# Optimization experiments

Hardware: AMD Instinct MI355X
Metric: run time of the kernel (lower is better)

Reference implementation:

```python
import jax, jax.numpy as jnp
import numpy as np

D_MODEL = 1024
EXPANSION = 4
NUM_TILES = 4
D_FF = D_MODEL * EXPANSION


def setup_inputs() -> dict:
    key = jax.random.key(0)
    k1, k2, k3, k4, k5 = jax.random.split(key, 5)
    x = jax.random.normal(k1, (8, 2048, D_MODEL), dtype=jnp.float32)
    w_up = jax.random.normal(k2, (D_FF, D_MODEL), dtype=jnp.float32) * 0.02
    b_up = jax.random.normal(k3, (D_FF,), dtype=jnp.float32) * 0.02
    w_down = jax.random.normal(k4, (D_MODEL, D_FF), dtype=jnp.float32) * 0.02
    b_down = jax.random.normal(k5, (D_MODEL,), dtype=jnp.float32) * 0.02
    return {"x": x, "w_up": w_up, "b_up": b_up, "w_down": w_down, "b_down": b_down}


def reference(x, w_up, b_up, w_down, b_down):
    B, T, C = x.shape
    xf = x.reshape(B * T, C)  # [N, d_model]
    N = B * T

    # Emergent tile signatures: sign of per-tile row sums of up_proj weight.
    tile_up = D_FF // NUM_TILES
    signatures = jnp.sign(w_up.reshape(NUM_TILES, tile_up, C).sum(axis=1))  # [num_tiles, d_model]

    # Routing: argmax over input-signature alignment -> one-hot gate.
    scores = xf @ signatures.T                      # [N, num_tiles]
    winner = jnp.argmax(scores, axis=-1)            # [N]
    gate = jax.nn.one_hot(winner, NUM_TILES, dtype=xf.dtype)  # [N, num_tiles]

    # Tile-gated up projection (gate scales output tile blocks), then ReLU.
    hidden = xf @ w_up.T + b_up                     # [N, d_ff]
    hidden = (hidden.reshape(N, NUM_TILES, tile_up) * gate[:, :, None]).reshape(N, D_FF)
    hidden = jax.nn.relu(hidden)

    # Tile-gated down projection.
    tile_down = D_MODEL // NUM_TILES
    out = hidden @ w_down.T + b_down                # [N, d_model]
    out = (out.reshape(N, NUM_TILES, tile_down) * gate[:, :, None]).reshape(N, D_MODEL)

    return out.reshape(B, T, D_MODEL), gate.reshape(B, T, NUM_TILES)
```

## Files before the change

kernel.cpp:

```cpp
#include <hip/hip_runtime.h>
#include <stdint.h>
#include <stddef.h>

#define N_TOK 16384
#define DM    1024
#define DFF   4096
#define NT    4
#define TU    1024
#define TD    256

typedef __attribute__((ext_vector_type(8))) short  short8;
typedef __attribute__((ext_vector_type(4))) short  short4v;
typedef __attribute__((ext_vector_type(4))) float  floatx4;

__device__ inline unsigned short f2bf(float f){
  union { float f; uint32_t u; } v; v.f = f;
  uint32_t u = v.u + 0x7FFFu + ((v.u >> 16) & 1u);
  return (unsigned short)(u >> 16);
}

__device__ __forceinline__ void gll16(const void* g, void* l){
  __builtin_amdgcn_global_load_lds(
      (const __attribute__((address_space(1))) unsigned int*)g,
      (__attribute__((address_space(3))) unsigned int*)l,
      16, 0, 0);
}

__global__ void k_sig_partial(const float* __restrict__ w_up,
                              float* __restrict__ partial,
                              unsigned short* __restrict__ wupb){
  const int b = blockIdx.x, tid = threadIdx.x;
  const int tile = b >> 6, chunk = b & 63;
  const int c0 = tid * 4;
  const int row0 = tile*TU + chunk*16;
  float s0=0.f, s1=0.f, s2=0.f, s3=0.f;
  const float* base = w_up + (size_t)row0 * DM + c0;
  #pragma unroll
  for (int r = 0; r < 16; ++r){
    floatx4 v = *(const floatx4*)(base + (size_t)r * DM);
    s0 += v[0]; s1 += v[1]; s2 += v[2]; s3 += v[3];
    short4v p;
    p[0]=(short)f2bf(v[0]); p[1]=(short)f2bf(v[1]);
    p[2]=(short)f2bf(v[2]); p[3]=(short)f2bf(v[3]);
    *(short4v*)(wupb + (size_t)(row0 + r) * DM + c0) = p;
  }
  float* p = partial + ((size_t)tile*DM + c0) * 64 + chunk;
  p[0] = s0; p[64] = s1; p[128] = s2; p[192] = s3;
}

__global__ void k_sig_final(const float* __restrict__ partial,
                            float* __restrict__ sig){
  const int g = blockIdx.x * 256 + threadIdx.x;
  const float* p = partial + (size_t)g * 64;
  float s = 0.f;
  #pragma unroll
  for (int i = 0; i < 64; ++i) s += p[i];
  sig[g] = (s > 0.f) ? 1.f : ((s < 0.f) ? -1.f : 0.f);
}

__global__ void k_wdown_conv(const float* __restrict__ w,
                             unsigned short* __restrict__ wb){
  const size_t i = ((size_t)blockIdx.x * 256 + threadIdx.x) * 8;
  floatx4 v0 = *(const floatx4*)(w + i);
  floatx4 v1 = *(const floatx4*)(w + i + 4);
  short8 p;
  p[0]=(short)f2bf(v0[0]); p[1]=(short)f2bf(v0[1]); p[2]=(short)f2bf(v0[2]); p[3]=(short)f2bf(v0[3]);
  p[4]=(short)f2bf(v1[0]); p[5]=(short)f2bf(v1[1]); p[6]=(short)f2bf(v1[2]); p[7]=(short)f2bf(v1[3]);
  *(short8*)(wb + i) = p;
}

__global__ __launch_bounds__(256) void k_route(
    const float* __restrict__ x, const float* __restrict__ sig,
    float* __restrict__ gate_out, int* __restrict__ winner,
    unsigned short* __restrict__ xbf){
  __shared__ float ssig[NT * DM];
  const int tid = threadIdx.x;
  for (int i = tid; i < NT*DM; i += 256) ssig[i] = sig[i];
  __syncthreads();
  const int wv = tid >> 6, lane = tid & 63;
  const int n = blockIdx.x * 4 + wv;
  const float* xr = x + (size_t)n * DM;
  unsigned short* xb = xbf + (size_t)n * 2048 + 1024;
  double a0=0.0, a1=0.0, a2=0.0, a3=0.0;
  #pragma unroll
  for (int j = 0; j < 4; ++j){
    const int c = j*256 + lane*4;
    floatx4 v = *(const floatx4*)(xr + c);
    short4v p;
    p[0]=(short)f2bf(v[0]); p[1]=(short)f2bf(v[1]);
    p[2]=(short)f2bf(v[2]); p[3]=(short)f2bf(v[3]);
    *(short4v*)(xb + c) = p;
    #pragma unroll
    for (int u = 0; u < 4; ++u){
      double xv = (double)v[u];
      a0 += xv * (double)ssig[c+u];
      a1 += xv * (double)ssig[DM   + c+u];
      a2 += xv * (double)ssig[2*DM + c+u];
      a3 += xv * (double)ssig[3*DM + c+u];
    }
  }
  #pragma unroll
  for (int off = 32; off > 0; off >>= 1){
    a0 += __shfl_down(a0, off, 64);
    a1 += __shfl_down(a1, off, 64);
    a2 += __shfl_down(a2, off, 64);
    a3 += __shfl_down(a3, off, 64);
  }
  if (lane == 0){
    double s[4] = {a0, a1, a2, a3};
    int w = 0;
    #pragma unroll
    for (int t = 1; t < 4; ++t) if (s[t] > s[w]) w = t;
    floatx4 g = { w==0 ? 1.f:0.f, w==1 ? 1.f:0.f, w==2 ? 1.f:0.f, w==3 ? 1.f:0.f };
    *(floatx4*)(gate_out + (size_t)n * 4) = g;
    winner[n] = w;
  }
}

__global__ void k_hist(const int* __restrict__ winner,
                       int* __restrict__ blk_cnt){
  __shared__ int wcnt[4][NT];
  const int tid = threadIdx.x, wv = tid >> 6, lane = tid & 63;
  const int w = winner[blockIdx.x * 256 + tid];
  #pragma unroll
  for (int t = 0; t < NT; ++t){
    unsigned long long m = __ballot(w == t);
    if (lane == 0) wcnt[wv][t] = __popcll(m);
  }
  __syncthreads();
  if (tid < NT){
    int s = wcnt[0][tid] + wcnt[1][tid] + wcnt[2][tid] + wcnt[3][tid];
    blk_cnt[blockIdx.x * NT + tid] = s;
  }
}

__global__ void k_scan(const int* __restrict__ blk_cnt,
                       int* __restrict__ meta, int* __restrict__ blk_base){
  __shared__ int s[256];
  const int tid = threadIdx.x;
  s[tid] = blk_cnt[tid];
  __syncthreads();
  if (tid == 0){
    int tot[NT] = {0,0,0,0};
    for (int b = 0; b < 64; ++b)
      for (int t = 0; t < NT; ++t) tot[t] += s[b*NT + t];
    int off = 0, base[NT];
    for (int t = 0; t < NT; ++t){ meta[t] = tot[t]; meta[4+t] = off; base[t] = off; off += tot[t]; }
    for (int b = 0; b < 64; ++b)
      for (int t = 0; t < NT; ++t){ int c = s[b*NT + t]; s[b*NT + t] = base[t]; base[t] += c; }
  }
  __syncthreads();
  blk_base[tid] = s[tid];
}

__global__ void k_scatter(const int* __restrict__ winner,
                          const int* __restrict__ blk_base,
                          int* __restrict__ idx){
  __shared__ int wcnt[4][NT];
  const int tid = threadIdx.x, wv = tid >> 6, lane = tid & 63;
  const int n = blockIdx.x * 256 + tid;
  const int w = winner[n];
  unsigned long long mymask = 0;
  #pragma unroll
  for (int t = 0; t < NT; ++t){
    unsigned long long m = __ballot(w == t);
    if (lane == 0) wcnt[wv][t] = __popcll(m);
    if (t == w) mymask = m;
  }
  __syncthreads();
  const unsigned long long below = (lane == 0) ? 0ull : (~0ull >> (64 - lane));
  int pos = blk_base[blockIdx.x * NT + w] + __popcll(mymask & below);
  for (int v = 0; v < wv; ++v) pos += wcnt[v][w];
  idx[pos] = n;
}

__global__ __launch_bounds__(256, 2) void k_gemm1(
    const unsigned short* __restrict__ xbf,
    const unsigned short* __restrict__ wupb,
    const float* __restrict__ b_up, const int* __restrict__ meta,
    const int* __restrict__ idx, unsigned short* __restrict__ hid){
  const int tile = blockIdx.z;
  const int cnt  = meta[tile];
  const int p0   = blockIdx.x * 128;
  if (p0 >= cnt) return;
  const int off  = meta[4 + tile];
  const int nb   = blockIdx.y;

  __shared__ unsigned short smem[16384];
  unsigned short* As0 = smem;
  unsigned short* As1 = smem + 4096;
  unsigned short* Bs0 = smem + 8192;
  unsigned short* Bs1 = smem + 12288;
  __shared__ int nrow[128];

  const int tid = threadIdx.x;
  if (tid < 128){
    int p = p0 + tid;
    nrow[tid] = idx[off + (p < cnt ? p : cnt - 1)];
  }
  __syncthreads();

  const int wv = tid >> 6, lane = tid & 63;
  const int wm = (wv >> 1) * 64, wn = (wv & 1) * 64;
  const int l16 = lane & 15, quad = lane >> 4;

  const int rsub = lane >> 2;
  const int kus  = (lane & 3) * 8;

  const int ra = wv*32 + rsub;
  const unsigned short* aptr0 = xbf + (size_t)nrow[ra]      * 2048 + 1024 + kus;
  const unsigned short* aptr1 = xbf + (size_t)nrow[ra + 16] * 2048 + 1024 + kus;
  const unsigned short* bptr0 = wupb + (size_t)(tile*TU + nb*128 + wv*32 + rsub) * DM + kus;
  const unsigned short* bptr1 = bptr0 + 16 * DM;

  unsigned short* a0d0 = As0 + (wv*32) * 32;  unsigned short* a0d1 = a0d0 + 16*32;
  unsigned short* a1d0 = As1 + (wv*32) * 32;  unsigned short* a1d1 = a1d0 + 16*32;
  unsigned short* b0d0 = Bs0 + (wv*32) * 32;  unsigned short* b0d1 = b0d0 + 16*32;
  unsigned short* b1d0 = Bs1 + (wv*32) * 32;  unsigned short* b1d1 = b1d0 + 16*32;

  floatx4 acc[4][4];
  #pragma unroll
  for (int i = 0; i < 4; ++i)
    #pragma unroll
    for (int j = 0; j < 4; ++j) acc[i][j] = (floatx4){0.f,0.f,0.f,0.f};

  for (int k0 = 0; k0 < DM; k0 += 64){
    gll16(aptr0 + k0,      a0d0);
    gll16(aptr1 + k0,      a0d1);
    gll16(aptr0 + k0 + 32, a1d0);
    gll16(aptr1 + k0 + 32, a1d1);
    gll16(bptr0 + k0,      b0d0);
    gll16(bptr1 + k0,      b0d1);
    gll16(bptr0 + k0 + 32, b1d0);
    gll16(bptr1 + k0 + 32, b1d1);
    __syncthreads();
    {
      short8 af[4], bfr[4];
      #pragma unroll
      for (int i = 0; i < 4; ++i) af[i]  = *(const short8*)(As0 + (wm + i*16 + l16)*32 + quad*8);
      #pragma unroll
      for (int j = 0; j < 4; ++j) bfr[j] = *(const short8*)(Bs0 + (wn + j*16 + l16)*32 + quad*8);
      #pragma unroll
      for (int i = 0; i < 4; ++i)
        #pragma unroll
        for (int j = 0; j < 4; ++j)
          acc[i][j] = __builtin_amdgcn_mfma_f32_16x16x32_bf16(af[i], bfr[j], acc[i][j], 0, 0, 0);
    }
    {
      short8 af[4], bfr[4];
      #pragma unroll
      for (int i = 0; i < 4; ++i) af[i]  = *(const short8*)(As1 + (wm + i*16 + l16)*32 + quad*8);
      #pragma unroll
      for (int j = 0; j < 4; ++j) bfr[j] = *(const short8*)(Bs1 + (wn + j*16 + l16)*32 + quad*8);
      #pragma unroll
      for (int i = 0; i < 4; ++i)
        #pragma unroll
        for (int j = 0; j < 4; ++j)
          acc[i][j] = __builtin_amdgcn_mfma_f32_16x16x32_bf16(af[i], bfr[j], acc[i][j], 0, 0, 0);
    }
    __syncthreads();
  }

  const int gcol0 = nb*128;
  #pragma unroll
  for (int half = 0; half < 2; ++half){
    if ((wv >> 1) == half){
      #pragma unroll
      for (int i = 0; i < 4; ++i){
        #pragma unroll
        for (int j = 0; j < 4; ++j){
          const int col = wn + j*16 + l16;
          const float bias = b_up[tile*TU + gcol0 + col];
          #pragma unroll
          for (int r = 0; r < 4; ++r){
            const int lrow = i*16 + quad*4 + r;
            float v = acc[i][j][r] + bias;
            smem[lrow*136 + col] = f2bf(v > 0.f ? v : 0.f);
          }
        }
      }
    }
    __syncthreads();
    #pragma unroll
    for (int c = tid; c < 1024; c += 256){
      const int lrow = c >> 4, k8 = (c & 15) * 8;
      const int m = half*64 + lrow;
      if (p0 + m < cnt){
        short8 vv = *(const short8*)(smem + lrow*136 + k8);
        *(short8*)(hid + (size_t)nrow[m]*2048 + gcol0 + k8) = vv;
      }
    }
    __syncthreads();
  }
}

__global__ __launch_bounds__(256, 2) void k_gemm2(
    const unsigned short* __restrict__ hid,
    const unsigned short* __restrict__ wdownb,
    const float* __restrict__ b_down, const int* __restrict__ meta,
    const int* __restrict__ idx, float* __restrict__ out){
  const int tile = blockIdx.z;
  const int cnt  = meta[tile];
  const int p0   = blockIdx.x * 32;
  if (p0 >= cnt) return;
  const int off  = meta[4 + tile];

  __shared__ unsigned short smem[18432];
  unsigned short* As0 = smem;
  unsigned short* As1 = smem + 1024;
  unsigned short* Bs0 = smem + 2048;
  unsigned short* Bs1 = smem + 10240;
  float* epi = (float*)smem;
  __shared__ int nrow[32];

  const int tid = threadIdx.x;
  if (tid < 32){
    int p = p0 + tid;
    nrow[tid] = idx[off + (p < cnt ? p : cnt - 1)];
  }
  __syncthreads();

  const int wv = tid >> 6, lane = tid & 63;
  const int wn = wv * 64;
  const int l16 = lane & 15, quad = lane >> 4;

  const int rsub = lane >> 2;
  const int kus  = (lane & 3) * 8;

  const int arow = (wv & 1)*16 + rsub;
  const unsigned short* aptr = hid + (size_t)nrow[arow] * 2048 + kus;
  const int aoff = (wv >> 1) * 32;
  unsigned short* asd = (wv < 2 ? As0 : As1) + ((wv & 1)*16) * 32;
  const unsigned short* bptr = wdownb + (size_t)(tile*TD + wv*64 + rsub) * DFF + tile*TU + kus;
  unsigned short* bsd0 = Bs0 + (wv*64) * 32;
  unsigned short* bsd1 = Bs1 + (wv*64) * 32;

  floatx4 acc[2][4];
  #pragma unroll
  for (int i = 0; i < 2; ++i)
    #pragma unroll
    for (int j = 0; j < 4; ++j) acc[i][j] = (floatx4){0.f,0.f,0.f,0.f};

  for (int k0 = 0; k0 < TU; k0 += 64){
    gll16(aptr + k0 + aoff, asd);
    gll16(bptr + k0,               bsd0);
    gll16(bptr + k0 + 16*DFF,      bsd0 + 16*32);
    gll16(bptr + k0 + 32*DFF,      bsd0 + 32*32);
    gll16(bptr + k0 + 48*DFF,      bsd0 + 48*32);
    gll16(bptr + k0 + 32,          bsd1);
    gll16(bptr + k0 + 32 + 16*DFF, bsd1 + 16*32);
    gll16(bptr + k0 + 32 + 32*DFF, bsd1 + 32*32);
    gll16(bptr + k0 + 32 + 48*DFF, bsd1 + 48*32);
    __syncthreads();
    {
      short8 af[2], bfr[4];
      #pragma unroll
      for (int i = 0; i < 2; ++i) af[i]  = *(const short8*)(As0 + (i*16 + l16)*32 + quad*8);
      #pragma unroll
      for (int j = 0; j < 4; ++j) bfr[j] = *(const short8*)(Bs0 + (wn + j*16 + l16)*32 + quad*8);
      #pragma unroll
      for (int i = 0; i < 2; ++i)
        #pragma unroll
        for (int j = 0; j < 4; ++j)
          acc[i][j] = __builtin_amdgcn_mfma_f32_16x16x32_bf16(af[i], bfr[j], acc[i][j], 0, 0, 0);
    }
    {
      short8 af[2], bfr[4];
      #pragma unroll
      for (int i = 0; i < 2; ++i) af[i]  = *(const short8*)(As1 + (i*16 + l16)*32 + quad*8);
      #pragma unroll
      for (int j = 0; j < 4; ++j) bfr[j] = *(const short8*)(Bs1 + (wn + j*16 + l16)*32 + quad*8);
      #pragma unroll
      for (int i = 0; i < 2; ++i)
        #pragma unroll
        for (int j = 0; j < 4; ++j)
          acc[i][j] = __builtin_amdgcn_mfma_f32_16x16x32_bf16(af[i], bfr[j], acc[i][j], 0, 0, 0);
    }
    __syncthreads();
  }

  const floatx4 z4 = {0.f, 0.f, 0.f, 0.f};
  #pragma unroll
  for (int cb = 0; cb < 4; ++cb){
    if (cb == tile) continue;
    for (int c = tid; c < 32*64; c += 256){
      const int rowl = c >> 6, c4 = (c & 63) * 4;
      if (p0 + rowl < cnt)
        *(floatx4*)(out + (size_t)nrow[rowl]*DM + cb*256 + c4) = z4;
    }
  }

  #pragma unroll
  for (int half = 0; half < 2; ++half){
    #pragma unroll
    for (int j = 0; j < 4; ++j){
      const int col = wn + j*16 + l16;
      const float bias = b_down[tile*TD + col];
      #pragma unroll
      for (int r = 0; r < 4; ++r){
        const int lrow = quad*4 + r;
        epi[lrow*260 + col] = acc[half][j][r] + bias;
      }
    }
    __syncthreads();
    #pragma unroll
    for (int c = tid; c < 1024; c += 256){
      const int lrow = c >> 6, c4 = (c & 63) * 4;
      const int m = half*16 + lrow;
      if (p0 + m < cnt){
        floatx4 v = *(const floatx4*)(epi + lrow*260 + c4);
        *(floatx4*)(out + (size_t)nrow[m]*DM + tile*TD + c4) = v;
      }
    }
    __syncthreads();
  }
}

extern "C" void kernel_launch(void* const* d_in, const int* in_sizes, int n_in,
                              void* d_out, int out_size, void* d_ws, size_t ws_size,
                              hipStream_t stream){
  const float* x      = (const float*)d_in[0];
  const float* w_up   = (const float*)d_in[1];
  const float* b_up   = (const float*)d_in[2];
  const float* w_down = (const float*)d_in[3];
  const float* b_down = (const float*)d_in[4];

  unsigned short* wupb   = (unsigned short*)d_ws;
  unsigned short* wdownb = wupb + (size_t)DFF * DM;
  float* partial = (float*)(wdownb + (size_t)DM * DFF);
  float* sig     = partial + 262144;
  int*   ints    = (int*)(sig + 4096);
  int*   winner   = ints;
  int*   idx      = ints + 16384;
  int*   meta     = ints + 32768;
  int*   blk_cnt  = ints + 32776;
  int*   blk_base = ints + 33032;

  float*          out  = (float*)d_out;
  float*          gate = out + (size_t)N_TOK * DM;
  unsigned short* ob16 = (unsigned short*)d_out;

  k_sig_partial<<<dim3(NT*64), 256, 0, stream>>>(w_up, partial, wupb);
  k_sig_final  <<<dim3(16),    256, 0, stream>>>(partial, sig);
  k_wdown_conv <<<dim3(2048),  256, 0, stream>>>(w_down, wdownb);
  k_route      <<<dim3(N_TOK/4), 256, 0, stream>>>(x, sig, gate, winner, ob16);
  k_hist       <<<dim3(64),    256, 0, stream>>>(winner, blk_cnt);
  k_scan       <<<dim3(1),     256, 0, stream>>>(blk_cnt, meta, blk_base);
  k_scatter    <<<dim3(64),    256, 0, stream>>>(winner, blk_base, idx);
  k_gemm1      <<<dim3(128, 8, NT), 256, 0, stream>>>(ob16, wupb, b_up, meta, idx, ob16);
  k_gemm2      <<<dim3(512, 1, NT), 256, 0, stream>>>(ob16, wdownb, b_down, meta, idx, out);
}
```

Before: 273.5 us.

## Fuse routing histogram/scan/scatter into route kernel via atomics and merge weight prep

New measurement: 274.0 us. No clear change (+0.2%).

```diff
diff --git a/kernel.cpp b/kernel.cpp
--- a/kernel.cpp
+++ b/kernel.cpp
@@ -26,10 +26,23 @@
       16, 0, 0);
 }
 
-__global__ void k_sig_partial(const float* __restrict__ w_up,
-                              float* __restrict__ partial,
-                              unsigned short* __restrict__ wupb){
-  const int b = blockIdx.x, tid = threadIdx.x;
+__global__ void k_prep(const float* __restrict__ w_up,
+                       const float* __restrict__ w_down,
+                       float* __restrict__ partial,
+                       unsigned short* __restrict__ wupb,
+                       unsigned short* __restrict__ wdownb){
+  const int tid = threadIdx.x;
+  if (blockIdx.x >= 256){
+    const size_t i = ((size_t)(blockIdx.x - 256) * 256 + tid) * 8;
+    floatx4 v0 = *(const floatx4*)(w_down + i);
+    floatx4 v1 = *(const floatx4*)(w_down + i + 4);
+    short8 p;
+    p[0]=(short)f2bf(v0[0]); p[1]=(short)f2bf(v0[1]); p[2]=(short)f2bf(v0[2]); p[3]=(short)f2bf(v0[3]);
+    p[4]=(short)f2bf(v1[0]); p[5]=(short)f2bf(v1[1]); p[6]=(short)f2bf(v1[2]); p[7]=(short)f2bf(v1[3]);
+    *(short8*)(wdownb + i) = p;
+    return;
+  }
+  const int b = blockIdx.x;
   const int tile = b >> 6, chunk = b & 63;
   const int c0 = tid * 4;
   const int row0 = tile*TU + chunk*16;
@@ -49,7 +62,9 @@
 }
 
 __global__ void k_sig_final(const float* __restrict__ partial,
-                            float* __restrict__ sig){
+                            float* __restrict__ sig,
+                            int* __restrict__ meta){
+  if (blockIdx.x == 0 && threadIdx.x < 8) meta[threadIdx.x] = 0;
   const int g = blockIdx.x * 256 + threadIdx.x;
   const float* p = partial + (size_t)g * 64;
   float s = 0.f;
@@ -58,132 +73,92 @@
   sig[g] = (s > 0.f) ? 1.f : ((s < 0.f) ? -1.f : 0.f);
 }
 
-__global__ void k_wdown_conv(const float* __restrict__ w,
-                             unsigned short* __restrict__ wb){
-  const size_t i = ((size_t)blockIdx.x * 256 + threadIdx.x) * 8;
-  floatx4 v0 = *(const floatx4*)(w + i);
-  floatx4 v1 = *(const floatx4*)(w + i + 4);
-  short8 p;
-  p[0]=(short)f2bf(v0[0]); p[1]=(short)f2bf(v0[1]); p[2]=(short)f2bf(v0[2]); p[3]=(short)f2bf(v0[3]);
-  p[4]=(short)f2bf(v1[0]); p[5]=(short)f2bf(v1[1]); p[6]=(short)f2bf(v1[2]); p[7]=(short)f2bf(v1[3]);
-  *(short8*)(wb + i) = p;
-}
-
 __global__ __launch_bounds__(256) void k_route(
     const float* __restrict__ x, const float* __restrict__ sig,
-    float* __restrict__ gate_out, int* __restrict__ winner,
-    unsigned short* __restrict__ xbf){
+    float* __restrict__ gate_out, int* __restrict__ meta,
+    int* __restrict__ idx4, unsigned short* __restrict__ xbf){
   __shared__ float ssig[NT * DM];
+  __shared__ int swin[16];
+  __shared__ int sbase[NT];
   const int tid = threadIdx.x;
   for (int i = tid; i < NT*DM; i += 256) ssig[i] = sig[i];
   __syncthreads();
   const int wv = tid >> 6, lane = tid & 63;
-  const int n = blockIdx.x * 4 + wv;
-  const float* xr = x + (size_t)n * DM;
-  unsigned short* xb = xbf + (size_t)n * 2048 + 1024;
-  double a0=0.0, a1=0.0, a2=0.0, a3=0.0;
+
+  floatx4 sg[4][4];
   #pragma unroll
   for (int j = 0; j < 4; ++j){
     const int c = j*256 + lane*4;
-    floatx4 v = *(const floatx4*)(xr + c);
-    short4v p;
-    p[0]=(short)f2bf(v[0]); p[1]=(short)f2bf(v[1]);
-    p[2]=(short)f2bf(v[2]); p[3]=(short)f2bf(v[3]);
-    *(short4v*)(xb + c) = p;
-    #pragma unroll
-    for (int u = 0; u < 4; ++u){
-      double xv = (double)v[u];
-      a0 += xv * (double)ssig[c+u];
-      a1 += xv * (double)ssig[DM   + c+u];
-      a2 += xv * (double)ssig[2*DM + c+u];
-      a3 += xv * (double)ssig[3*DM + c+u];
-    }
-  }
-  #pragma unroll
-  for (int off = 32; off > 0; off >>= 1){
-    a0 += __shfl_down(a0, off, 64);
-    a1 += __shfl_down(a1, off, 64);
-    a2 += __shfl_down(a2, off, 64);
-    a3 += __shfl_down(a3, off, 64);
-  }
-  if (lane == 0){
-    double s[4] = {a0, a1, a2, a3};
-    int w = 0;
-    #pragma unroll
-    for (int t = 1; t < 4; ++t) if (s[t] > s[w]) w = t;
-    floatx4 g = { w==0 ? 1.f:0.f, w==1 ? 1.f:0.f, w==2 ? 1.f:0.f, w==3 ? 1.f:0.f };
-    *(floatx4*)(gate_out + (size_t)n * 4) = g;
-    winner[n] = w;
-  }
-}
-
-__global__ void k_hist(const int* __restrict__ winner,
-                       int* __restrict__ blk_cnt){
-  __shared__ int wcnt[4][NT];
-  const int tid = threadIdx.x, wv = tid >> 6, lane = tid & 63;
-  const int w = winner[blockIdx.x * 256 + tid];
-  #pragma unroll
-  for (int t = 0; t < NT; ++t){
-    unsigned long long m = __ballot(w == t);
-    if (lane == 0) wcnt[wv][t] = __popcll(m);
+    #pragma unroll
+    for (int tt = 0; tt < 4; ++tt)
+      sg[j][tt] = *(const floatx4*)(ssig + tt*DM + c);
+  }
+
+  #pragma unroll
+  for (int t = 0; t < 4; ++t){
+    const int n = blockIdx.x * 16 + wv * 4 + t;
+    const float* xr = x + (size_t)n * DM;
+    unsigned short* xb = xbf + (size_t)n * 2048 + 1024;
+    double a0=0.0, a1=0.0, a2=0.0, a3=0.0;
+    #pragma unroll
+    for (int j = 0; j < 4; ++j){
+      const int c = j*256 + lane*4;
+      floatx4 v = *(const floatx4*)(xr + c);
+      short4v p;
+      p[0]=(short)f2bf(v[0]); p[1]=(short)f2bf(v[1]);
+      p[2]=(short)f2bf(v[2]); p[3]=(short)f2bf(v[3]);
+      *(short4v*)(xb + c) = p;
+      #pragma unroll
+      for (int u = 0; u < 4; ++u){
+        double xv = (double)v[u];
+        a0 += xv * (double)sg[j][0][u];
+        a1 += xv * (double)sg[j][1][u];
+        a2 += xv * (double)sg[j][2][u];
+        a3 += xv * (double)sg[j][3][u];
+      }
+    }
+    #pragma unroll
+    for (int off = 32; off > 0; off >>= 1){
+      a0 += __shfl_down(a0, off, 64);
+      a1 += __shfl_down(a1, off, 64);
+      a2 += __shfl_down(a2, off, 64);
+      a3 += __shfl_down(a3, off, 64);
+    }
+    if (lane == 0){
+      double s[4] = {a0, a1, a2, a3};
+      int w = 0;
+      #pragma unroll
+      for (int tt = 1; tt < 4; ++tt) if (s[tt] > s[w]) w = tt;
+      floatx4 g = { w==0 ? 1.f:0.f, w==1 ? 1.f:0.f, w==2 ? 1.f:0.f, w==3 ? 1.f:0.f };
+      *(floatx4*)(gate_out + (size_t)n * 4) = g;
+      swin[wv*4 + t] = w;
+    }
   }
   __syncthreads();
   if (tid < NT){
-    int s = wcnt[0][tid] + wcnt[1][tid] + wcnt[2][tid] + wcnt[3][tid];
-    blk_cnt[blockIdx.x * NT + tid] = s;
-  }
-}
-
-__global__ void k_scan(const int* __restrict__ blk_cnt,
-                       int* __restrict__ meta, int* __restrict__ blk_base){
-  __shared__ int s[256];
-  const int tid = threadIdx.x;
-  s[tid] = blk_cnt[tid];
+    int c = 0;
+    #pragma unroll
+    for (int i = 0; i < 16; ++i) c += (swin[i] == tid) ? 1 : 0;
+    sbase[tid] = atomicAdd(&meta[tid], c);
+  }
   __syncthreads();
-  if (tid == 0){
-    int tot[NT] = {0,0,0,0};
-    for (int b = 0; b < 64; ++b)
-      for (int t = 0; t < NT; ++t) tot[t] += s[b*NT + t];
-    int off = 0, base[NT];
-    for (int t = 0; t < NT; ++t){ meta[t] = tot[t]; meta[4+t] = off; base[t] = off; off += tot[t]; }
-    for (int b = 0; b < 64; ++b)
-      for (int t = 0; t < NT; ++t){ int c = s[b*NT + t]; s[b*NT + t] = base[t]; base[t] += c; }
-  }
-  __syncthreads();
-  blk_base[tid] = s[tid];
-}
-
-__global__ void k_scatter(const int* __restrict__ winner,
-                          const int* __restrict__ blk_base,
-                          int* __restrict__ idx){
-  __shared__ int wcnt[4][NT];
-  const int tid = threadIdx.x, wv = tid >> 6, lane = tid & 63;
-  const int n = blockIdx.x * 256 + tid;
-  const int w = winner[n];
-  unsigned long long mymask = 0;
-  #pragma unroll
-  for (int t = 0; t < NT; ++t){
-    unsigned long long m = __ballot(w == t);
-    if (lane == 0) wcnt[wv][t] = __popcll(m);
-    if (t == w) mymask = m;
-  }
-  __syncthreads();
-  const unsigned long long below = (lane == 0) ? 0ull : (~0ull >> (64 - lane));
-  int pos = blk_base[blockIdx.x * NT + w] + __popcll(mymask & below);
-  for (int v = 0; v < wv; ++v) pos += wcnt[v][w];
-  idx[pos] = n;
+  if (tid < 16){
+    const int w = swin[tid];
+    int r = 0;
+    for (int i = 0; i < tid; ++i) r += (swin[i] == w) ? 1 : 0;
+    idx4[w * N_TOK + sbase[w] + r] = blockIdx.x * 16 + tid;
+  }
 }
 
 __global__ __launch_bounds__(256, 2) void k_gemm1(
     const unsigned short* __restrict__ xbf,
     const unsigned short* __restrict__ wupb,
     const float* __restrict__ b_up, const int* __restrict__ meta,
-    const int* __restrict__ idx, unsigned short* __restrict__ hid){
+    const int* __restrict__ idx4, unsigned short* __restrict__ hid){
   const int tile = blockIdx.z;
   const int cnt  = meta[tile];
   const int p0   = blockIdx.x * 128;
   if (p0 >= cnt) return;
-  const int off  = meta[4 + tile];
   const int nb   = blockIdx.y;
 
   __shared__ unsigned short smem[16384];
@@ -196,7 +171,7 @@
   const int tid = threadIdx.x;
   if (tid < 128){
     int p = p0 + tid;
-    nrow[tid] = idx[off + (p < cnt ? p : cnt - 1)];
+    nrow[tid] = idx4[tile * N_TOK + (p < cnt ? p : cnt - 1)];
   }
   __syncthreads();
 
@@ -298,12 +273,11 @@
     const unsigned short* __restrict__ hid,
     const unsigned short* __restrict__ wdownb,
     const float* __restrict__ b_down, const int* __restrict__ meta,
-    const int* __restrict__ idx, float* __restrict__ out){
+    const int* __restrict__ idx4, float* __restrict__ out){
   const int tile = blockIdx.z;
   const int cnt  = meta[tile];
   const int p0   = blockIdx.x * 32;
   if (p0 >= cnt) return;
-  const int off  = meta[4 + tile];
 
   __shared__ unsigned short smem[18432];
   unsigned short* As0 = smem;
@@ -316,7 +290,7 @@
   const int tid = threadIdx.x;
   if (tid < 32){
     int p = p0 + tid;
-    nrow[tid] = idx[off + (p < cnt ? p : cnt - 1)];
+    nrow[tid] = idx4[tile * N_TOK + (p < cnt ? p : cnt - 1)];
   }
   __syncthreads();
 
@@ -429,24 +403,16 @@
   unsigned short* wdownb = wupb + (size_t)DFF * DM;
   float* partial = (float*)(wdownb + (size_t)DM * DFF);
   float* sig     = partial + 262144;
-  int*   ints    = (int*)(sig + 4096);
-  int*   winner   = ints;
-  int*   idx      = ints + 16384;
-  int*   meta     = ints + 32768;
-  int*   blk_cnt  = ints + 32776;
-  int*   blk_base = ints + 33032;
+  int*   meta    = (int*)(sig + 4096);
+  int*   idx4    = (int*)partial;
 
   float*          out  = (float*)d_out;
   float*          gate = out + (size_t)N_TOK * DM;
   unsigned short* ob16 = (unsigned short*)d_out;
 
-  k_sig_partial<<<dim3(NT*64), 256, 0, stream>>>(w_up, partial, wupb);
-  k_sig_final  <<<dim3(16),    256, 0, stream>>>(partial, sig);
-  k_wdown_conv <<<dim3(2048),  256, 0, stream>>>(w_down, wdownb);
-  k_route      <<<dim3(N_TOK/4), 256, 0, stream>>>(x, sig, gate, winner, ob16);
-  k_hist       <<<dim3(64),    256, 0, stream>>>(winner, blk_cnt);
-  k_scan       <<<dim3(1),     256, 0, stream>>>(blk_cnt, meta, blk_base);
-  k_scatter    <<<dim3(64),    256, 0, stream>>>(winner, blk_base, idx);
-  k_gemm1      <<<dim3(128, 8, NT), 256, 0, stream>>>(ob16, wupb, b_up, meta, idx, ob16);
-  k_gemm2      <<<dim3(512, 1, NT), 256, 0, stream>>>(ob16, wdownb, b_down, meta, idx, out);
-}
+  k_prep      <<<dim3(2304), 256, 0, stream>>>(w_up, w_down, partial, wupb, wdownb);
+  k_sig_final <<<dim3(16),   256, 0, stream>>>(partial, sig, meta);
+  k_route     <<<dim3(N_TOK/16), 256, 0, stream>>>(x, sig, gate, meta, idx4, ob16);
+  k_gemm1     <<<dim3(128, 8, NT), 256, 0, stream>>>(ob16, wupb, b_up, meta, idx4, ob16);
+  k_gemm2     <<<dim3(512, 1, NT), 256, 0, stream>>>(ob16, wdownb, b_down, meta, idx4, out);
+}
```
